# Performance work log

Hardware: AMD Instinct MI355X
Metric: run time of the kernel (lower is better)

Reference implementation:

```python
import jax, jax.numpy as jnp
import numpy as np

B, T, C, H = 2, 2048, 1024, 16
HS = C // H  # head size = 64


def setup_inputs() -> dict:
    key = jax.random.key(0)
    k1, k2, k3 = jax.random.split(key, 3)
    X = jax.random.normal(k1, (B, T, C), dtype=jnp.float32)
    W_qkv = jax.random.normal(k2, (C, 3 * C), dtype=jnp.float32) * (C ** -0.5)
    W_proj = jax.random.normal(k3, (C, C), dtype=jnp.float32) * (C ** -0.5)
    return {"X": X, "W_qkv": W_qkv, "W_proj": W_proj}


def reference(X, W_qkv, W_proj):
    b, t, c = X.shape
    h, hs = H, c // H
    qkv = X @ W_qkv                      # [b,t,3c]
    k_, q_, v_ = jnp.split(qkv, 3, axis=2)  # module order: K, Q, V
    K = k_.reshape(b, t, h, hs).transpose(0, 2, 1, 3)  # [b,h,t,hs]
    Q = q_.reshape(b, t, h, hs).transpose(0, 2, 1, 3)
    V = v_.reshape(b, t, h, hs).transpose(0, 2, 1, 3)
    # NOTE: original scales by full embed dim c**-0.5 (not head_size)
    scores = jnp.einsum('bhqd,bhkd->bhqk', Q, K) * (c ** -0.5)
    causal = jnp.tril(jnp.ones((t, t), dtype=bool))
    scores = jnp.where(causal, scores, -jnp.inf)
    W = jax.nn.softmax(scores, axis=-1)  # dropout is identity in eval mode
    out = jnp.einsum('bhqk,bhkd->bhqd', W, V)  # [b,h,t,hs]
    out = out.transpose(0, 2, 1, 3).reshape(b, t, c)
    return out @ W_proj
```

## Files before the change

kernel.cpp:

```cpp
#include <hip/hip_runtime.h>

#define TB 2
#define TT 2048
#define TC 1024
#define TH 16
#define THS 64

typedef short bf16x8 __attribute__((ext_vector_type(8)));
typedef float f32x4 __attribute__((ext_vector_type(4)));

#define QSCALE 0.0450842200278f

__device__ inline unsigned short f2b(float f) {
    unsigned u = __builtin_bit_cast(unsigned, f);
    unsigned r = (u + 0x7fffu + ((u >> 16) & 1u)) >> 16;
    return (unsigned short)r;
}

__device__ inline void gl_lds16(const unsigned short* g, unsigned short* l) {
    __builtin_amdgcn_global_load_lds(
        (const __attribute__((address_space(1))) unsigned int*)(g),
        (__attribute__((address_space(3))) unsigned int*)(l), 16, 0, 0);
}

__device__ inline float dpp_sum16(float x) {
    int t;
    t = __builtin_amdgcn_update_dpp(0, __builtin_bit_cast(int, x), 0x128, 0xf, 0xf, true);
    x += __builtin_bit_cast(float, t);
    t = __builtin_amdgcn_update_dpp(0, __builtin_bit_cast(int, x), 0x124, 0xf, 0xf, true);
    x += __builtin_bit_cast(float, t);
    t = __builtin_amdgcn_update_dpp(0, __builtin_bit_cast(int, x), 0x122, 0xf, 0xf, true);
    x += __builtin_bit_cast(float, t);
    t = __builtin_amdgcn_update_dpp(0, __builtin_bit_cast(int, x), 0x121, 0xf, 0xf, true);
    x += __builtin_bit_cast(float, t);
    return x;
}

__global__ void cvt_bf16_k(const float* __restrict__ in, unsigned short* __restrict__ out) {
    const int i = blockIdx.x * blockDim.x + threadIdx.x;
    const float4* p = (const float4*)in + (size_t)i * 2;
    const float4 a = p[0], b = p[1];
    bf16x8 v;
    v[0] = (short)f2b(a.x); v[1] = (short)f2b(a.y);
    v[2] = (short)f2b(a.z); v[3] = (short)f2b(a.w);
    v[4] = (short)f2b(b.x); v[5] = (short)f2b(b.y);
    v[6] = (short)f2b(b.z); v[7] = (short)f2b(b.w);
    *(bf16x8*)(out + (size_t)i * 8) = v;
}

__global__ void transpose_cvt_k(const float* __restrict__ in,
                                unsigned short* __restrict__ out, int R, int Cc) {
    __shared__ float tile[32][33];
    const int tx = threadIdx.x, ty = threadIdx.y;
    const int r0 = blockIdx.y * 32, c0 = blockIdx.x * 32;
#pragma unroll
    for (int i = 0; i < 4; i++)
        tile[ty + i * 8][tx] = in[(size_t)(r0 + ty + i * 8) * Cc + c0 + tx];
    __syncthreads();
#pragma unroll
    for (int i = 0; i < 4; i++)
        out[(size_t)(c0 + ty + i * 8) * R + r0 + tx] = f2b(tile[tx][ty + i * 8]);
}

__global__ void vt_k(const unsigned short* __restrict__ Vb,
                     unsigned short* __restrict__ Vt) {
    __shared__ unsigned short tile[32][33];
    const int tx = threadIdx.x, ty = threadIdx.y;
    const int d0 = blockIdx.x * 32, t0 = blockIdx.y * 32, bh = blockIdx.z;
    const unsigned short* src = Vb + (size_t)bh * TT * THS;
    unsigned short* dst = Vt + (size_t)bh * THS * TT;
#pragma unroll
    for (int i = 0; i < 4; i++)
        tile[ty + i * 8][tx] = src[(size_t)(t0 + ty + i * 8) * THS + d0 + tx];
    __syncthreads();
#pragma unroll
    for (int i = 0; i < 4; i++)
        dst[(size_t)(d0 + ty + i * 8) * TT + t0 + tx] = tile[tx][ty + i * 8];
}

__global__ __launch_bounds__(256) void gemm_qkv(
    const unsigned short* __restrict__ A, const unsigned short* __restrict__ Bt, int K,
    unsigned short* __restrict__ outK, unsigned short* __restrict__ outQ,
    unsigned short* __restrict__ outV) {
    __shared__ __align__(16) unsigned short As[128 * 32];
    __shared__ __align__(16) unsigned short Bs[128 * 32];

    const int tid = threadIdx.x;
    const int wave = tid >> 6, lane = tid & 63;
    const int quad = lane >> 4, l16 = lane & 15;
    const int wm = (wave >> 1) * 64, wn = (wave & 1) * 64;
    const int m0 = blockIdx.y * 128, n0 = blockIdx.x * 128;

    const f32x4 vzero = {0.f, 0.f, 0.f, 0.f};
    f32x4 acc[4][4];
#pragma unroll
    for (int i = 0; i < 4; i++)
#pragma unroll
        for (int j = 0; j < 4; j++) acc[i][j] = vzero;

    const int nk = K >> 5;
    for (int kt = 0; kt < nk; ++kt) {
        const int k0 = kt * 32;
        __syncthreads();
#pragma unroll
        for (int it = 0; it < 2; ++it) {
            const int chunk = tid + it * 256;
            const int r = chunk >> 2, col = (chunk & 3) * 8;
            gl_lds16(A + (size_t)(m0 + r) * K + k0 + col, &As[chunk * 8]);
            gl_lds16(Bt + (size_t)(n0 + r) * K + k0 + col, &Bs[chunk * 8]);
        }
        __syncthreads();
        bf16x8 af[4], bfr[4];
#pragma unroll
        for (int f = 0; f < 4; ++f) {
            af[f] = *(const bf16x8*)(&As[(wm + f * 16 + l16) * 32 + quad * 8]);
            bfr[f] = *(const bf16x8*)(&Bs[(wn + f * 16 + l16) * 32 + quad * 8]);
        }
#pragma unroll
        for (int fm = 0; fm < 4; ++fm)
#pragma unroll
            for (int fn = 0; fn < 4; ++fn)
                acc[fm][fn] = __builtin_amdgcn_mfma_f32_16x16x32_bf16(
                    af[fm], bfr[fn], acc[fm][fn], 0, 0, 0);
    }

#pragma unroll
    for (int fm = 0; fm < 4; ++fm) {
#pragma unroll
        for (int fn = 0; fn < 4; ++fn) {
#pragma unroll
            for (int r = 0; r < 4; ++r) {
                const int row = m0 + wm + fm * 16 + quad * 4 + r;
                const int col = n0 + wn + fn * 16 + l16;
                const float val = acc[fm][fn][r];
                const int b = row >> 11, t = row & (TT - 1);
                const int chunkc = col >> 10, cc = col & (TC - 1);
                const int hh = cc >> 6, d = cc & 63;
                const size_t idx = (size_t)((b * TH + hh) * TT + t) * THS + d;
                if (chunkc == 0)
                    outK[idx] = f2b(val);
                else if (chunkc == 1)
                    outQ[idx] = f2b(val * QSCALE);
                else
                    outV[idx] = f2b(val);
            }
        }
    }
}

__global__ __launch_bounds__(256) void gemm_proj(
    const unsigned short* __restrict__ A, const unsigned short* __restrict__ Bt,
    int M, int N, int K, float* __restrict__ outF) {
    __shared__ __align__(16) unsigned short As[128 * 32];
    __shared__ __align__(16) unsigned short Bs[64 * 32];

    const int tid = threadIdx.x;
    const int wave = tid >> 6, lane = tid & 63;
    const int quad = lane >> 4, l16 = lane & 15;
    const int wm = wave * 32;
    const int m0 = blockIdx.y * 128, n0 = blockIdx.x * 64;

    const f32x4 vzero = {0.f, 0.f, 0.f, 0.f};
    f32x4 acc[2][4];
#pragma unroll
    for (int i = 0; i < 2; i++)
#pragma unroll
        for (int j = 0; j < 4; j++) acc[i][j] = vzero;

    const int nk = K >> 5;
    for (int kt = 0; kt < nk; ++kt) {
        const int k0 = kt * 32;
        __syncthreads();
#pragma unroll
        for (int it = 0; it < 2; ++it) {
            const int chunk = tid + it * 256;
            const int r = chunk >> 2, col = (chunk & 3) * 8;
            gl_lds16(A + (size_t)(m0 + r) * K + k0 + col, &As[chunk * 8]);
        }
        {
            const int r = tid >> 2, col = (tid & 3) * 8;
            gl_lds16(Bt + (size_t)(n0 + r) * K + k0 + col, &Bs[tid * 8]);
        }
        __syncthreads();
        bf16x8 af[2], bfr[4];
#pragma unroll
        for (int f = 0; f < 2; ++f)
            af[f] = *(const bf16x8*)(&As[(wm + f * 16 + l16) * 32 + quad * 8]);
#pragma unroll
        for (int f = 0; f < 4; ++f)
            bfr[f] = *(const bf16x8*)(&Bs[(f * 16 + l16) * 32 + quad * 8]);
#pragma unroll
        for (int fm = 0; fm < 2; ++fm)
#pragma unroll
            for (int fn = 0; fn < 4; ++fn)
                acc[fm][fn] = __builtin_amdgcn_mfma_f32_16x16x32_bf16(
                    af[fm], bfr[fn], acc[fm][fn], 0, 0, 0);
    }

#pragma unroll
    for (int fm = 0; fm < 2; ++fm)
#pragma unroll
        for (int fn = 0; fn < 4; ++fn)
#pragma unroll
            for (int r = 0; r < 4; ++r) {
                const int row = m0 + wm + fm * 16 + quad * 4 + r;
                const int col = n0 + fn * 16 + l16;
                outF[(size_t)row * N + col] = acc[fm][fn][r];
            }
}

__global__ __launch_bounds__(256, 3) void attn_k(
    const unsigned short* __restrict__ Qb, const unsigned short* __restrict__ Kb,
    const unsigned short* __restrict__ Vt, unsigned short* __restrict__ AO) {
    __shared__ __align__(16) float U[4][2112];
    __shared__ float lS[4][32];

    const int tid = threadIdx.x;
    const int w = tid >> 6, lane = tid & 63;
    const int quad = lane >> 4, l16 = lane & 15;
    const int bh = blockIdx.x;
    const int qtt = 63 - blockIdx.y;
    const int q0 = qtt * 32;
    const unsigned short* Qh = Qb + (size_t)bh * TT * THS;
    const unsigned short* Kh = Kb + (size_t)bh * TT * THS;
    const unsigned short* Vh = Vt + (size_t)bh * THS * TT;

    bf16x8 aQ[2][2];
#pragma unroll
    for (int rt = 0; rt < 2; ++rt)
#pragma unroll
        for (int ks = 0; ks < 2; ++ks)
            aQ[rt][ks] = *(const bf16x8*)(
                Qh + (size_t)(q0 + rt * 16 + l16) * THS + ks * 32 + quad * 8);

    const float NEGINF = -__builtin_inff();
    const f32x4 vzero = {0.f, 0.f, 0.f, 0.f};
    f32x4 o[2][4];
    float lp[2][4];
#pragma unroll
    for (int rt = 0; rt < 2; ++rt)
#pragma unroll
        for (int i = 0; i < 4; i++) { o[rt][i] = vzero; lp[rt][i] = 0.f; }

    const int nkt = (qtt >> 1) + 1;
    for (int kt = w; kt < nkt; kt += 4) {
        const int t0 = kt * 64;
        bf16x8 bK[8], bV[8];
#pragma unroll
        for (int nt = 0; nt < 4; ++nt)
#pragma unroll
            for (int ks = 0; ks < 2; ++ks) {
                bK[nt * 2 + ks] = *(const bf16x8*)(
                    Kh + (size_t)(t0 + nt * 16 + l16) * THS + ks * 32 + quad * 8);
                bV[nt * 2 + ks] = *(const bf16x8*)(
                    Vh + (size_t)(nt * 16 + l16) * TT + t0 + ks * 32 + quad * 8);
            }
        const bool needmask = (kt == nkt - 1);
#pragma unroll
        for (int rt = 0; rt < 2; ++rt) {
            f32x4 s[4];
#pragma unroll
            for (int nt = 0; nt < 4; ++nt) s[nt] = vzero;
#pragma unroll
            for (int ks = 0; ks < 2; ++ks)
#pragma unroll
                for (int nt = 0; nt < 4; ++nt)
                    s[nt] = __builtin_amdgcn_mfma_f32_16x16x32_bf16(
                        aQ[rt][ks], bK[nt * 2 + ks], s[nt], 0, 0, 0);
            unsigned short* Pw = (unsigned short*)&U[w][0] + rt * 1152;
#pragma unroll
            for (int r = 0; r < 4; ++r) {
                const int row = q0 + rt * 16 + quad * 4 + r;
                float v0 = s[0][r], v1 = s[1][r], v2 = s[2][r], v3 = s[3][r];
                if (needmask) {
                    if (t0 + l16 > row) v0 = NEGINF;
                    if (t0 + 16 + l16 > row) v1 = NEGINF;
                    if (t0 + 32 + l16 > row) v2 = NEGINF;
                    if (t0 + 48 + l16 > row) v3 = NEGINF;
                }
                const float p0 = __builtin_amdgcn_exp2f(v0);
                const float p1 = __builtin_amdgcn_exp2f(v1);
                const float p2 = __builtin_amdgcn_exp2f(v2);
                const float p3 = __builtin_amdgcn_exp2f(v3);
                lp[rt][r] += (p0 + p1) + (p2 + p3);
                const int pr = (quad * 4 + r) * 72;
                Pw[pr + l16] = f2b(p0);
                Pw[pr + 16 + l16] = f2b(p1);
                Pw[pr + 32 + l16] = f2b(p2);
                Pw[pr + 48 + l16] = f2b(p3);
            }
            asm volatile("s_waitcnt lgkmcnt(0)" ::: "memory");
            bf16x8 aP[2];
            aP[0] = *(const bf16x8*)(Pw + l16 * 72 + quad * 8);
            aP[1] = *(const bf16x8*)(Pw + l16 * 72 + 32 + quad * 8);
#pragma unroll
            for (int ks = 0; ks < 2; ++ks)
#pragma unroll
                for (int nt = 0; nt < 4; ++nt)
                    o[rt][nt] = __builtin_amdgcn_mfma_f32_16x16x32_bf16(
                        aP[ks], bV[nt * 2 + ks], o[rt][nt], 0, 0, 0);
        }
    }

#pragma unroll
    for (int rt = 0; rt < 2; ++rt)
#pragma unroll
        for (int r = 0; r < 4; ++r) {
            const float lsum = dpp_sum16(lp[rt][r]);
            const int row = rt * 16 + quad * 4 + r;
            if (l16 == 0) lS[w][row] = lsum;
#pragma unroll
            for (int nt = 0; nt < 4; ++nt)
                U[w][row * 66 + nt * 16 + l16] = o[rt][nt][r];
        }
    __syncthreads();

    const int b = bh >> 4, h = bh & 15;
    const int col = w * 16 + l16;
#pragma unroll
    for (int rr = 0; rr < 8; ++rr) {
        const int row = quad * 8 + rr;
        const float L = (lS[0][row] + lS[1][row]) + (lS[2][row] + lS[3][row]);
        const float O = (U[0][row * 66 + col] + U[1][row * 66 + col]) +
                        (U[2][row * 66 + col] + U[3][row * 66 + col]);
        const int t = q0 + row;
        AO[((size_t)(b * TT + t)) * TC + h * 64 + col] = f2b(O / L);
    }
}

extern "C" void kernel_launch(void* const* d_in, const int* in_sizes, int n_in,
                              void* d_out, int out_size, void* d_ws, size_t ws_size,
                              hipStream_t stream) {
    const float* X = (const float*)d_in[0];
    const float* Wqkv = (const float*)d_in[1];
    const float* Wproj = (const float*)d_in[2];
    float* out = (float*)d_out;

    unsigned short* ws = (unsigned short*)d_ws;
    unsigned short* Xb = ws;
    unsigned short* Wq_t = Xb + 4096 * 1024;
    unsigned short* Wp_t = Wq_t + 3072 * 1024;
    unsigned short* Qb = Wp_t + 1024 * 1024;
    unsigned short* Kb = Qb + TB * TH * TT * THS;
    unsigned short* Vb = Kb + TB * TH * TT * THS;
    unsigned short* Vt = Vb + TB * TH * TT * THS;
    unsigned short* AO = Vt + TB * TH * TT * THS;

    cvt_bf16_k<<<dim3((4096 * 1024) / (8 * 256)), 256, 0, stream>>>(X, Xb);
    transpose_cvt_k<<<dim3(3072 / 32, 1024 / 32), dim3(32, 8), 0, stream>>>(Wqkv, Wq_t, 1024, 3072);
    transpose_cvt_k<<<dim3(1024 / 32, 1024 / 32), dim3(32, 8), 0, stream>>>(Wproj, Wp_t, 1024, 1024);
    gemm_qkv<<<dim3(3072 / 128, 4096 / 128), 256, 0, stream>>>(Xb, Wq_t, 1024, Kb, Qb, Vb);
    vt_k<<<dim3(THS / 32, TT / 32, TB * TH), dim3(32, 8), 0, stream>>>(Vb, Vt);
    attn_k<<<dim3(32, 64), 256, 0, stream>>>(Qb, Kb, Vt, AO);
    gemm_proj<<<dim3(1024 / 64, 4096 / 128), 256, 0, stream>>>(
        AO, Wp_t, 4096, 1024, 1024, out);
}
```

Baseline: 215.5 us.

## Shrink attention LDS to bf16 and batch P reloads across row tiles

```diff
diff --git a/kernel.cpp b/kernel.cpp
--- a/kernel.cpp
+++ b/kernel.cpp
@@ -15,6 +15,10 @@
     unsigned u = __builtin_bit_cast(unsigned, f);
     unsigned r = (u + 0x7fffu + ((u >> 16) & 1u)) >> 16;
     return (unsigned short)r;
+}
+__device__ inline float b2f(unsigned short h) {
+    unsigned u = ((unsigned)h) << 16;
+    return __builtin_bit_cast(float, u);
 }
 
 __device__ inline void gl_lds16(const unsigned short* g, unsigned short* l) {
@@ -212,7 +216,7 @@
 __global__ __launch_bounds__(256, 3) void attn_k(
     const unsigned short* __restrict__ Qb, const unsigned short* __restrict__ Kb,
     const unsigned short* __restrict__ Vt, unsigned short* __restrict__ AO) {
-    __shared__ __align__(16) float U[4][2112];
+    __shared__ __align__(16) unsigned short U[4][2304];
     __shared__ float lS[4][32];
 
     const int tid = threadIdx.x;
@@ -267,7 +271,7 @@
                 for (int nt = 0; nt < 4; ++nt)
                     s[nt] = __builtin_amdgcn_mfma_f32_16x16x32_bf16(
                         aQ[rt][ks], bK[nt * 2 + ks], s[nt], 0, 0, 0);
-            unsigned short* Pw = (unsigned short*)&U[w][0] + rt * 1152;
+            unsigned short* Pw = &U[w][0] + rt * 1152;
 #pragma unroll
             for (int r = 0; r < 4; ++r) {
                 const int row = q0 + rt * 16 + quad * 4 + r;
@@ -289,17 +293,23 @@
                 Pw[pr + 32 + l16] = f2b(p2);
                 Pw[pr + 48 + l16] = f2b(p3);
             }
-            asm volatile("s_waitcnt lgkmcnt(0)" ::: "memory");
-            bf16x8 aP[2];
-            aP[0] = *(const bf16x8*)(Pw + l16 * 72 + quad * 8);
-            aP[1] = *(const bf16x8*)(Pw + l16 * 72 + 32 + quad * 8);
+        }
+        asm volatile("s_waitcnt lgkmcnt(0)" ::: "memory");
+        bf16x8 aP[2][2];
+#pragma unroll
+        for (int rt = 0; rt < 2; ++rt) {
+            const unsigned short* Pw = &U[w][0] + rt * 1152;
+            aP[rt][0] = *(const bf16x8*)(Pw + l16 * 72 + quad * 8);
+            aP[rt][1] = *(const bf16x8*)(Pw + l16 * 72 + 32 + quad * 8);
+        }
+#pragma unroll
+        for (int rt = 0; rt < 2; ++rt)
 #pragma unroll
             for (int ks = 0; ks < 2; ++ks)
 #pragma unroll
                 for (int nt = 0; nt < 4; ++nt)
                     o[rt][nt] = __builtin_amdgcn_mfma_f32_16x16x32_bf16(
-                        aP[ks], bV[nt * 2 + ks], o[rt][nt], 0, 0, 0);
-        }
+                        aP[rt][ks], bV[nt * 2 + ks], o[rt][nt], 0, 0, 0);
     }
 
 #pragma unroll
@@ -311,7 +321,7 @@
             if (l16 == 0) lS[w][row] = lsum;
 #pragma unroll
             for (int nt = 0; nt < 4; ++nt)
-                U[w][row * 66 + nt * 16 + l16] = o[rt][nt][r];
+                U[w][row * 66 + nt * 16 + l16] = f2b(o[rt][nt][r]);
         }
     __syncthreads();
 
@@ -321,10 +331,10 @@
     for (int rr = 0; rr < 8; ++rr) {
         const int row = quad * 8 + rr;
         const float L = (lS[0][row] + lS[1][row]) + (lS[2][row] + lS[3][row]);
-        const float O = (U[0][row * 66 + col] + U[1][row * 66 + col]) +
-                        (U[2][row * 66 + col] + U[3][row * 66 + col]);
+        const float O = (b2f(U[0][row * 66 + col]) + b2f(U[1][row * 66 + col])) +
+                        (b2f(U[2][row * 66 + col]) + b2f(U[3][row * 66 + col]));
         const int t = q0 + row;
-        AO[((size_t)(b * TT + t)) * TC + h * 64 + col] = f2b(O / L);
+        AO[((size_t)(b * TT + t)) * TC + h * 64 + col] = f2b(O * __builtin_amdgcn_rcpf(L));
     }
 }
 
```

New measurement: 213.5 us. No clear change (-0.9%).

## Compute transposed scores so P stays in registers, skipping the LDS round-trip

Applied to the files above, without the earlier changes.

```diff
diff --git a/kernel.cpp b/kernel.cpp
--- a/kernel.cpp
+++ b/kernel.cpp
@@ -7,6 +7,7 @@
 #define THS 64
 
 typedef short bf16x8 __attribute__((ext_vector_type(8)));
+typedef short bf16x4 __attribute__((ext_vector_type(4)));
 typedef float f32x4 __attribute__((ext_vector_type(4)));
 
 #define QSCALE 0.0450842200278f
@@ -21,19 +22,6 @@
     __builtin_amdgcn_global_load_lds(
         (const __attribute__((address_space(1))) unsigned int*)(g),
         (__attribute__((address_space(3))) unsigned int*)(l), 16, 0, 0);
-}
-
-__device__ inline float dpp_sum16(float x) {
-    int t;
-    t = __builtin_amdgcn_update_dpp(0, __builtin_bit_cast(int, x), 0x128, 0xf, 0xf, true);
-    x += __builtin_bit_cast(float, t);
-    t = __builtin_amdgcn_update_dpp(0, __builtin_bit_cast(int, x), 0x124, 0xf, 0xf, true);
-    x += __builtin_bit_cast(float, t);
-    t = __builtin_amdgcn_update_dpp(0, __builtin_bit_cast(int, x), 0x122, 0xf, 0xf, true);
-    x += __builtin_bit_cast(float, t);
-    t = __builtin_amdgcn_update_dpp(0, __builtin_bit_cast(int, x), 0x121, 0xf, 0xf, true);
-    x += __builtin_bit_cast(float, t);
-    return x;
 }
 
 __global__ void cvt_bf16_k(const float* __restrict__ in, unsigned short* __restrict__ out) {
@@ -209,10 +197,10 @@
             }
 }
 
-__global__ __launch_bounds__(256, 3) void attn_k(
+__global__ __launch_bounds__(256, 2) void attn_k(
     const unsigned short* __restrict__ Qb, const unsigned short* __restrict__ Kb,
     const unsigned short* __restrict__ Vt, unsigned short* __restrict__ AO) {
-    __shared__ __align__(16) float U[4][2112];
+    __shared__ float U[4][32 * 66];
     __shared__ float lS[4][32];
 
     const int tid = threadIdx.x;
@@ -236,95 +224,94 @@
     const float NEGINF = -__builtin_inff();
     const f32x4 vzero = {0.f, 0.f, 0.f, 0.f};
     f32x4 o[2][4];
-    float lp[2][4];
+    float lp[2] = {0.f, 0.f};
 #pragma unroll
     for (int rt = 0; rt < 2; ++rt)
 #pragma unroll
-        for (int i = 0; i < 4; i++) { o[rt][i] = vzero; lp[rt][i] = 0.f; }
+        for (int i = 0; i < 4; i++) o[rt][i] = vzero;
 
     const int nkt = (qtt >> 1) + 1;
     for (int kt = w; kt < nkt; kt += 4) {
         const int t0 = kt * 64;
-        bf16x8 bK[8], bV[8];
+        bf16x8 bK[4][2];
 #pragma unroll
         for (int nt = 0; nt < 4; ++nt)
 #pragma unroll
-            for (int ks = 0; ks < 2; ++ks) {
-                bK[nt * 2 + ks] = *(const bf16x8*)(
+            for (int ks = 0; ks < 2; ++ks)
+                bK[nt][ks] = *(const bf16x8*)(
                     Kh + (size_t)(t0 + nt * 16 + l16) * THS + ks * 32 + quad * 8);
-                bV[nt * 2 + ks] = *(const bf16x8*)(
-                    Vh + (size_t)(nt * 16 + l16) * TT + t0 + ks * 32 + quad * 8);
+        f32x4 s[2][4];
+#pragma unroll
+        for (int rt = 0; rt < 2; ++rt)
+#pragma unroll
+            for (int nt = 0; nt < 4; ++nt) s[rt][nt] = vzero;
+#pragma unroll
+        for (int ks = 0; ks < 2; ++ks)
+#pragma unroll
+            for (int rt = 0; rt < 2; ++rt)
+#pragma unroll
+                for (int nt = 0; nt < 4; ++nt)
+                    s[rt][nt] = __builtin_amdgcn_mfma_f32_16x16x32_bf16(
+                        bK[nt][ks], aQ[rt][ks], s[rt][nt], 0, 0, 0);
+        bf16x4 bV[4][4];
+#pragma unroll
+        for (int nt = 0; nt < 4; ++nt)
+#pragma unroll
+            for (int ntd = 0; ntd < 4; ++ntd)
+                bV[nt][ntd] = *(const bf16x4*)(
+                    Vh + (size_t)(ntd * 16 + l16) * TT + t0 + nt * 16 + quad * 4);
+        const bool needmask = (kt == nkt - 1);
+        bf16x4 Pp[2][4];
+#pragma unroll
+        for (int rt = 0; rt < 2; ++rt) {
+            const int q = q0 + rt * 16 + l16;
+#pragma unroll
+            for (int nt = 0; nt < 4; ++nt) {
+                float p[4];
+#pragma unroll
+                for (int r = 0; r < 4; ++r) {
+                    float v = s[rt][nt][r];
+                    if (needmask && (t0 + nt * 16 + quad * 4 + r > q)) v = NEGINF;
+                    p[r] = __builtin_amdgcn_exp2f(v);
+                }
+                lp[rt] += (p[0] + p[1]) + (p[2] + p[3]);
+                bf16x4 pk;
+                pk[0] = (short)f2b(p[0]); pk[1] = (short)f2b(p[1]);
+                pk[2] = (short)f2b(p[2]); pk[3] = (short)f2b(p[3]);
+                Pp[rt][nt] = pk;
             }
-        const bool needmask = (kt == nkt - 1);
-#pragma unroll
-        for (int rt = 0; rt < 2; ++rt) {
-            f32x4 s[4];
-#pragma unroll
-            for (int nt = 0; nt < 4; ++nt) s[nt] = vzero;
-#pragma unroll
-            for (int ks = 0; ks < 2; ++ks)
-#pragma unroll
-                for (int nt = 0; nt < 4; ++nt)
-                    s[nt] = __builtin_amdgcn_mfma_f32_16x16x32_bf16(
-                        aQ[rt][ks], bK[nt * 2 + ks], s[nt], 0, 0, 0);
-            unsigned short* Pw = (unsigned short*)&U[w][0] + rt * 1152;
-#pragma unroll
-            for (int r = 0; r < 4; ++r) {
-                const int row = q0 + rt * 16 + quad * 4 + r;
-                float v0 = s[0][r], v1 = s[1][r], v2 = s[2][r], v3 = s[3][r];
-                if (needmask) {
-                    if (t0 + l16 > row) v0 = NEGINF;
-                    if (t0 + 16 + l16 > row) v1 = NEGINF;
-                    if (t0 + 32 + l16 > row) v2 = NEGINF;
-                    if (t0 + 48 + l16 > row) v3 = NEGINF;
-                }
-                const float p0 = __builtin_amdgcn_exp2f(v0);
-                const float p1 = __builtin_amdgcn_exp2f(v1);
-                const float p2 = __builtin_amdgcn_exp2f(v2);
-                const float p3 = __builtin_amdgcn_exp2f(v3);
-                lp[rt][r] += (p0 + p1) + (p2 + p3);
-                const int pr = (quad * 4 + r) * 72;
-                Pw[pr + l16] = f2b(p0);
-                Pw[pr + 16 + l16] = f2b(p1);
-                Pw[pr + 32 + l16] = f2b(p2);
-                Pw[pr + 48 + l16] = f2b(p3);
-            }
-            asm volatile("s_waitcnt lgkmcnt(0)" ::: "memory");
-            bf16x8 aP[2];
-            aP[0] = *(const bf16x8*)(Pw + l16 * 72 + quad * 8);
-            aP[1] = *(const bf16x8*)(Pw + l16 * 72 + 32 + quad * 8);
-#pragma unroll
-            for (int ks = 0; ks < 2; ++ks)
-#pragma unroll
-                for (int nt = 0; nt < 4; ++nt)
-                    o[rt][nt] = __builtin_amdgcn_mfma_f32_16x16x32_bf16(
-                        aP[ks], bV[nt * 2 + ks], o[rt][nt], 0, 0, 0);
-        }
-    }
-
-#pragma unroll
-    for (int rt = 0; rt < 2; ++rt)
-#pragma unroll
-        for (int r = 0; r < 4; ++r) {
-            const float lsum = dpp_sum16(lp[rt][r]);
-            const int row = rt * 16 + quad * 4 + r;
-            if (l16 == 0) lS[w][row] = lsum;
-#pragma unroll
-            for (int nt = 0; nt < 4; ++nt)
-                U[w][row * 66 + nt * 16 + l16] = o[rt][nt][r];
-        }
+        }
+#pragma unroll
+        for (int nt = 0; nt < 4; ++nt)
+#pragma unroll
+            for (int rt = 0; rt < 2; ++rt)
+#pragma unroll
+                for (int ntd = 0; ntd < 4; ++ntd)
+                    o[rt][ntd] = __builtin_amdgcn_mfma_f32_16x16x16bf16_1k(
+                        bV[nt][ntd], Pp[rt][nt], o[rt][ntd], 0, 0, 0);
+    }
+
+#pragma unroll
+    for (int rt = 0; rt < 2; ++rt) {
+        lp[rt] += __shfl_xor(lp[rt], 16);
+        lp[rt] += __shfl_xor(lp[rt], 32);
+        if (quad == 0) lS[w][rt * 16 + l16] = lp[rt];
+#pragma unroll
+        for (int ntd = 0; ntd < 4; ++ntd)
+#pragma unroll
+            for (int r = 0; r < 4; ++r)
+                U[w][(rt * 16 + l16) * 66 + ntd * 16 + quad * 4 + r] = o[rt][ntd][r];
+    }
     __syncthreads();
 
     const int b = bh >> 4, h = bh & 15;
-    const int col = w * 16 + l16;
-#pragma unroll
-    for (int rr = 0; rr < 8; ++rr) {
-        const int row = quad * 8 + rr;
-        const float L = (lS[0][row] + lS[1][row]) + (lS[2][row] + lS[3][row]);
-        const float O = (U[0][row * 66 + col] + U[1][row * 66 + col]) +
-                        (U[2][row * 66 + col] + U[3][row * 66 + col]);
-        const int t = q0 + row;
-        AO[((size_t)(b * TT + t)) * TC + h * 64 + col] = f2b(O / L);
+#pragma unroll
+    for (int i = 0; i < 8; ++i) {
+        const int q = w * 8 + i;
+        const float L = (lS[0][q] + lS[1][q]) + (lS[2][q] + lS[3][q]);
+        const float O = (U[0][q * 66 + lane] + U[1][q * 66 + lane]) +
+                        (U[2][q * 66 + lane] + U[3][q * 66 + lane]);
+        AO[((size_t)(b * TT + q0 + q)) * TC + h * 64 + lane] = f2b(O / L);
     }
 }
 
```

New measurement: 246.5 us. 14.4% more time.
